# Kernel tuning notes

Measured on AMD Instinct MI355X. Metric: run time of the kernel, lower is better.

## Reference

```python
import jax, jax.numpy as jnp
import numpy as np

TOP_K = 64   # make_graph default top_k
KMIN = 9     # make_graph default kmin
EPS = 1e-6


def rbf(D):
    # matches rbf(): D_min=0, D_max=20, D_count=36
    D_mu = jnp.linspace(0.0, 20.0, 36)
    D_sigma = 20.0 / 36
    return jnp.exp(-(((D[..., None] - D_mu) / D_sigma) ** 2))


def setup_inputs() -> dict:
    key = jax.random.key(0)
    ks = jax.random.split(key, 6)
    B, L, E, Dn, Do = 1, 1536, 32, 32, 32
    # backbone coords (B, L, 3 atoms, 3); scaled so CA-CA distances span the RBF range
    xyz = jax.random.normal(ks[0], (B, L, 3, 3), jnp.float32) * 10.0
    pair = jax.random.normal(ks[1], (B, L, L, E), jnp.float32)   # embedded pair feats (num_edge_features)
    node = jax.random.normal(ks[2], (B, L, Dn), jnp.float32)      # l0 node features
    idx = jnp.broadcast_to(jnp.arange(L, dtype=jnp.int32), (B, L))  # residue indices
    W_e = jax.random.normal(ks[3], (E + 36, Do), jnp.float32) / np.sqrt(E + 36)
    W_n = jax.random.normal(ks[4], (Dn, Do), jnp.float32) / np.sqrt(Dn)
    w_gate = jax.random.normal(ks[5], (Do,), jnp.float32) / np.sqrt(Do)
    return {"xyz": xyz, "pair": pair, "node": node, "idx": idx,
            "W_e": W_e, "W_n": W_n, "w_gate": w_gate}


def reference(xyz, pair, node, idx, W_e, W_n, w_gate):
    B, L = xyz.shape[:2]
    ca = xyz[:, :, 1]                                   # (B,L,3) CA coords
    diff = ca[:, None, :, :] - ca[:, :, None, :]        # d_ij = ca_j - ca_i  (B,L,L,3)
    D = jnp.sqrt(jnp.sum(diff * diff, -1) + 1e-12)      # cdist (B,L,L)
    eye = jnp.eye(L, dtype=D.dtype)
    D_big = D + eye[None] * 999.9                       # mask self for kNN, as in make_graph
    sep = jnp.abs(idx[:, None, :] - idx[:, :, None]).astype(D.dtype) + eye[None] * 999.9

    # topk smallest distances -> scatter into dense adjacency, union with seq-sep < kmin
    k = min(TOP_K, L)
    _, E_idx = jax.lax.top_k(-D_big, k)                 # (B,L,k)
    topk = jnp.zeros((B, L, L), D.dtype).at[
        jnp.arange(B)[:, None, None], jnp.arange(L)[None, :, None], E_idx].set(1.0)
    mask = jnp.logical_or(topk > 0.0, sep < KMIN)       # (B,L,L) graph edges

    # per-edge features: pair feats ++ 36-dim RBF of CA distance
    edge_feat = jnp.concatenate([pair, rbf(D)], -1)     # (B,L,L,E+36)
    msg = jax.nn.relu(
        jnp.einsum('bijf,fo->bijo', edge_feat, W_e)
        + jnp.einsum('bjd,do->bjo', node, W_n)[:, None, :, :])
    msg = msg * mask[..., None]
    deg = jnp.sum(mask.astype(msg.dtype), -1, keepdims=True)   # (B,L,1)

    node_out = jnp.sum(msg, 2) / (deg + EPS)            # (B,L,Do) scalar output
    gate = jnp.einsum('bijo,o->bij', msg, w_gate)       # per-edge scalar gate
    # edge vectors are detached in make_graph (edata['d'] = (...).detach())
    diff_sg = jax.lax.stop_gradient(diff)
    vec_out = jnp.sum(gate[..., None] * diff_sg, 2) / (deg + EPS)  # (B,L,3) vector output
    return jnp.concatenate([node_out, vec_out], -1)     # (B,L,Do+3)
```

## Files before the change

kernel.cpp:

```cpp
#include <hip/hip_runtime.h>
#include <hip/hip_bf16.h>
#include <math.h>

#define L_MAX 1536
#define TOPK  64
#define KMIN  9

__launch_bounds__(256, 2)
__global__ void finalblock_kernel(
    const float* __restrict__ xyz,
    const float* __restrict__ pair,
    const float* __restrict__ node,
    const int*   __restrict__ idxg,
    const float* __restrict__ We,
    const float* __restrict__ Wn,
    const float* __restrict__ wg,
    float* __restrict__ out,
    int B, int L)
{
    const int tid = threadIdx.x;
    const int row = blockIdx.x;
    const int b = row / L;
    const int i = row - b * L;

    __shared__ float    ca[L_MAX * 3];
    __shared__ unsigned d2b[L_MAX];
    __shared__ float    We_s[68 * 32];
    __shared__ float    Wn_s[32 * 32];
    __shared__ float    wg_s[32];
    __shared__ float    feat[8][100];
    __shared__ int      elist[128];
    __shared__ float    red[8 * 32];
    __shared__ float    vred[8][3];
    __shared__ int      ecnt;
    __shared__ int      wsum[4];

    for (int t = tid; t < 68 * 32; t += 256) We_s[t] = We[t];
    for (int t = tid; t < 32 * 32; t += 256) Wn_s[t] = Wn[t];
    if (tid < 32) wg_s[tid] = wg[tid];
    for (int t = tid; t < L * 3; t += 256) {
        int j = t / 3, c = t - j * 3;
        ca[t] = xyz[((size_t)(b * L + j)) * 9 + 3 + c];
    }
    if (tid == 0) ecnt = 0;
    __syncthreads();

    const float cix = ca[i * 3 + 0], ciy = ca[i * 3 + 1], ciz = ca[i * 3 + 2];

    for (int j = tid; j < L; j += 256) {
        float dx = ca[j * 3 + 0] - cix;
        float dy = ca[j * 3 + 1] - ciy;
        float dz = ca[j * 3 + 2] - ciz;
        float d2 = dx * dx + dy * dy + dz * dz + 1e-12f;
        if (j == i) d2 = 3.0e38f;
        d2b[j] = __float_as_uint(d2);
    }
    __syncthreads();

    unsigned v[6];
    unsigned char alive = 0;
    int nv = 0;
    for (int j = tid; j < L; j += 256) { v[nv] = d2b[j]; alive |= (unsigned char)(1u << nv); nv++; }

    unsigned thr = 0;
    int kk = TOPK;
    for (int bit = 31; bit >= 0; --bit) {
        int cnt = 0; unsigned char c0 = 0;
        for (int e = 0; e < nv; e++) {
            if ((alive >> e) & 1) {
                if (!((v[e] >> bit) & 1u)) { c0 |= (unsigned char)(1u << e); cnt++; }
            }
        }
        for (int off = 32; off; off >>= 1) cnt += __shfl_xor(cnt, off, 64);
        if ((tid & 63) == 0) wsum[tid >> 6] = cnt;
        __syncthreads();
        int C = wsum[0] + wsum[1] + wsum[2] + wsum[3];
        __syncthreads();
        if (C >= kk) {
            alive &= c0;
        } else {
            kk -= C;
            alive = (unsigned char)(alive & ~c0);
            thr |= (1u << bit);
        }
    }

    const int idx_i = idxg[b * L + i];
    for (int j = tid; j < L; j += 256) {
        bool m = (d2b[j] <= thr);
        if (!m && j != i) {
            int s = idxg[b * L + j] - idx_i;
            s = s < 0 ? -s : s;
            m = (s < KMIN);
        }
        if (m) {
            int p = atomicAdd(&ecnt, 1);
            if (p < 128) elist[p] = j;
        }
    }
    __syncthreads();
    const int deg = ecnt < 128 ? ecnt : 128;

    const int slot = tid >> 5;
    const int o    = tid & 31;
    float node_acc = 0.f;
    float vx = 0.f, vy = 0.f, vz = 0.f;

    for (int base = 0; base < deg; base += 8) {
        __syncthreads();
        const int eg = base + slot;

        if (eg < deg) {
            int j = elist[eg];
            feat[slot][o]      = pair[((size_t)(b * L + i) * L + j) * 32 + o];
            feat[slot][68 + o] = node[((size_t)(b * L + j)) * 32 + o];
        } else {
            feat[slot][o] = 0.f;
            feat[slot][68 + o] = 0.f;
        }
        for (int q = tid; q < 8 * 36; q += 256) {
            int sl = q / 36, r = q - sl * 36;
            int eg2 = base + sl;
            float val = 0.f;
            if (eg2 < deg) {
                float Dv = sqrtf(__uint_as_float(d2b[elist[eg2]]));
                float t = (Dv - (float)r * (20.0f / 35.0f)) * (36.0f / 20.0f);
                val = __expf(-t * t);
            }
            feat[sl][32 + r] = val;
        }
        __syncthreads();

        float acc = 0.f;
        if (eg < deg) {
            #pragma unroll
            for (int f = 0; f < 68; f++) acc = fmaf(feat[slot][f], We_s[f * 32 + o], acc);
            #pragma unroll
            for (int d = 0; d < 32; d++) acc = fmaf(feat[slot][68 + d], Wn_s[d * 32 + o], acc);
            acc = fmaxf(acc, 0.f);
        }
        node_acc += acc;

        float g = acc * wg_s[o];
        for (int w = 16; w; w >>= 1) g += __shfl_xor(g, w, 32);
        if (o == 0 && eg < deg) {
            int j = elist[eg];
            vx += g * (ca[j * 3 + 0] - cix);
            vy += g * (ca[j * 3 + 1] - ciy);
            vz += g * (ca[j * 3 + 2] - ciz);
        }
    }

    red[slot * 32 + o] = node_acc;
    if (o == 0) { vred[slot][0] = vx; vred[slot][1] = vy; vred[slot][2] = vz; }
    __syncthreads();

    const float denom = (float)deg + 1e-6f;
    const size_t orow = (size_t)(b * L + i) * 35;
    if (tid < 32) {
        float s = 0.f;
        #pragma unroll
        for (int s8 = 0; s8 < 8; s8++) s += red[s8 * 32 + tid];
        out[orow + tid] = s / denom;
    } else if (tid < 35) {
        int c = tid - 32;
        float s = 0.f;
        #pragma unroll
        for (int s8 = 0; s8 < 8; s8++) s += vred[s8][c];
        out[orow + 32 + c] = s / denom;
    }
}

extern "C" void kernel_launch(void* const* d_in, const int* in_sizes, int n_in,
                              void* d_out, int out_size, void* d_ws, size_t ws_size,
                              hipStream_t stream) {
    const float* xyz  = (const float*)d_in[0];
    const float* pair = (const float*)d_in[1];
    const float* node = (const float*)d_in[2];
    const int*   idx  = (const int*)d_in[3];
    const float* We   = (const float*)d_in[4];
    const float* Wn   = (const float*)d_in[5];
    const float* wg   = (const float*)d_in[6];
    float* out = (float*)d_out;

    const int BL = in_sizes[3];
    const long pair_sz = (long)in_sizes[1];
    const int L = (int)(pair_sz / ((long)BL * 32));
    const int B = BL / L;

    finalblock_kernel<<<dim3(B * L), dim3(256), 0, stream>>>(
        xyz, pair, node, idx, We, Wn, wg, out, B, L);
}
```

Baseline: 464.0 us.

## Process one row per wavefront with ballot-based radix top-k and register weights

Each 256-thread block now handles four rows, one wavefront per row, instead of one row per block. The radix select uses wave ballots with no block barriers and exits early once the remaining candidates exactly fill k. The edge list is built by ballot prefix instead of shared atomics, weights are held in registers, and the next edge's features are prefetched during compute. The cost is heavy register pressure from the 100-float weight column plus 24 distance values. The per-row state also assumes all four rows in a block share the same batch index.

```diff
diff --git a/kernel.cpp b/kernel.cpp
--- a/kernel.cpp
+++ b/kernel.cpp
@@ -5,6 +5,9 @@
 #define L_MAX 1536
 #define TOPK  64
 #define KMIN  9
+#define RPB   4
+#define NV    24
+#define MAXE  128
 
 __launch_bounds__(256, 2)
 __global__ void finalblock_kernel(
@@ -18,156 +21,206 @@
     float* __restrict__ out,
     int B, int L)
 {
-    const int tid = threadIdx.x;
-    const int row = blockIdx.x;
-    const int b = row / L;
-    const int i = row - b * L;
-
-    __shared__ float    ca[L_MAX * 3];
-    __shared__ unsigned d2b[L_MAX];
-    __shared__ float    We_s[68 * 32];
-    __shared__ float    Wn_s[32 * 32];
-    __shared__ float    wg_s[32];
-    __shared__ float    feat[8][100];
-    __shared__ int      elist[128];
-    __shared__ float    red[8 * 32];
-    __shared__ float    vred[8][3];
-    __shared__ int      ecnt;
-    __shared__ int      wsum[4];
-
-    for (int t = tid; t < 68 * 32; t += 256) We_s[t] = We[t];
-    for (int t = tid; t < 32 * 32; t += 256) Wn_s[t] = Wn[t];
-    if (tid < 32) wg_s[tid] = wg[tid];
+    const int tid  = threadIdx.x;
+    const int lane = tid & 63;
+    const int w    = tid >> 6;
+    const int row  = blockIdx.x * RPB + w;
+    const int BL   = B * L;
+
+    __shared__ float ca[L_MAX * 3];
+    __shared__ alignas(16) float feat[RPB][2][104];
+    __shared__ int   elist[RPB][MAXE];
+    __shared__ float ed2[RPB][MAXE];
+
+    const int b0 = (blockIdx.x * RPB) / L;
     for (int t = tid; t < L * 3; t += 256) {
         int j = t / 3, c = t - j * 3;
-        ca[t] = xyz[((size_t)(b * L + j)) * 9 + 3 + c];
-    }
-    if (tid == 0) ecnt = 0;
+        ca[t] = xyz[((size_t)(b0 * L + j)) * 9 + 3 + c];
+    }
     __syncthreads();
 
-    const float cix = ca[i * 3 + 0], ciy = ca[i * 3 + 1], ciz = ca[i * 3 + 2];
-
-    for (int j = tid; j < L; j += 256) {
-        float dx = ca[j * 3 + 0] - cix;
-        float dy = ca[j * 3 + 1] - ciy;
-        float dz = ca[j * 3 + 2] - ciz;
-        float d2 = dx * dx + dy * dy + dz * dz + 1e-12f;
-        if (j == i) d2 = 3.0e38f;
-        d2b[j] = __float_as_uint(d2);
-    }
-    __syncthreads();
-
-    unsigned v[6];
-    unsigned char alive = 0;
-    int nv = 0;
-    for (int j = tid; j < L; j += 256) { v[nv] = d2b[j]; alive |= (unsigned char)(1u << nv); nv++; }
-
-    unsigned thr = 0;
+    if (row >= BL) return;
+    const int i = row - b0 * L;
+    const int gbase = b0 * L;
+    const int o = lane & 31;
+    const int e2 = lane >> 5;
+
+    const float ci0 = ca[i * 3 + 0], ci1 = ca[i * 3 + 1], ci2 = ca[i * 3 + 2];
+
+    unsigned vbits[NV];
+    unsigned aliveInit = 0u;
+    #pragma unroll
+    for (int t = 0; t < NV; ++t) {
+        int j = lane + (t << 6);
+        unsigned ub = 0x7F7FFFFFu;
+        if (j < L) {
+            float dx = ca[j * 3 + 0] - ci0;
+            float dy = ca[j * 3 + 1] - ci1;
+            float dz = ca[j * 3 + 2] - ci2;
+            float d2 = dx * dx + dy * dy + dz * dz + 1e-12f;
+            if (j == i) d2 = 3.0e38f;
+            ub = __float_as_uint(d2);
+            aliveInit |= (1u << t);
+        }
+        vbits[t] = ub;
+    }
+
+    unsigned thr = 0u;
+    unsigned alive = aliveInit;
     int kk = TOPK;
-    for (int bit = 31; bit >= 0; --bit) {
-        int cnt = 0; unsigned char c0 = 0;
-        for (int e = 0; e < nv; e++) {
-            if ((alive >> e) & 1) {
-                if (!((v[e] >> bit) & 1u)) { c0 |= (unsigned char)(1u << e); cnt++; }
-            }
-        }
-        for (int off = 32; off; off >>= 1) cnt += __shfl_xor(cnt, off, 64);
-        if ((tid & 63) == 0) wsum[tid >> 6] = cnt;
-        __syncthreads();
-        int C = wsum[0] + wsum[1] + wsum[2] + wsum[3];
-        __syncthreads();
-        if (C >= kk) {
-            alive &= c0;
-        } else {
-            kk -= C;
-            alive = (unsigned char)(alive & ~c0);
-            thr |= (1u << bit);
-        }
-    }
-
-    const int idx_i = idxg[b * L + i];
-    for (int j = tid; j < L; j += 256) {
-        bool m = (d2b[j] <= thr);
-        if (!m && j != i) {
-            int s = idxg[b * L + j] - idx_i;
-            s = s < 0 ? -s : s;
-            m = (s < KMIN);
-        }
+    int aliveCnt = L;
+    for (int bit = 30; bit >= 0; --bit) {
+        unsigned c0 = 0u;
+        int cnt = 0;
+        #pragma unroll
+        for (int t = 0; t < NV; ++t) {
+            bool z = ((alive >> t) & 1u) && !((vbits[t] >> bit) & 1u);
+            unsigned long long blt = __ballot((int)z);
+            cnt += __popcll(blt);
+            if (z) c0 |= (1u << t);
+        }
+        if (cnt >= kk) { alive &= c0; aliveCnt = cnt; }
+        else { kk -= cnt; aliveCnt -= cnt; alive &= ~c0; thr |= (1u << bit); }
+        if (aliveCnt == kk) {
+            unsigned mx = 0u;
+            #pragma unroll
+            for (int t = 0; t < NV; ++t)
+                if ((alive >> t) & 1u) mx = vbits[t] > mx ? vbits[t] : mx;
+            #pragma unroll
+            for (int off = 32; off; off >>= 1) {
+                unsigned m2 = (unsigned)__shfl_xor((int)mx, off, 64);
+                mx = m2 > mx ? m2 : mx;
+            }
+            thr = mx;
+            break;
+        }
+    }
+
+    const int idx_i = idxg[gbase + i];
+    int cnt = 0;
+    #pragma unroll
+    for (int t = 0; t < NV; ++t) {
+        int j = lane + (t << 6);
+        bool m = false;
+        if (j < L) {
+            m = (vbits[t] <= thr);
+            if (!m && j != i) {
+                int s = idxg[gbase + j] - idx_i;
+                s = s < 0 ? -s : s;
+                m = (s < KMIN);
+            }
+        }
+        unsigned long long blt = __ballot((int)m);
         if (m) {
-            int p = atomicAdd(&ecnt, 1);
-            if (p < 128) elist[p] = j;
-        }
-    }
-    __syncthreads();
-    const int deg = ecnt < 128 ? ecnt : 128;
-
-    const int slot = tid >> 5;
-    const int o    = tid & 31;
-    float node_acc = 0.f;
-    float vx = 0.f, vy = 0.f, vz = 0.f;
-
-    for (int base = 0; base < deg; base += 8) {
-        __syncthreads();
-        const int eg = base + slot;
-
-        if (eg < deg) {
-            int j = elist[eg];
-            feat[slot][o]      = pair[((size_t)(b * L + i) * L + j) * 32 + o];
-            feat[slot][68 + o] = node[((size_t)(b * L + j)) * 32 + o];
-        } else {
-            feat[slot][o] = 0.f;
-            feat[slot][68 + o] = 0.f;
-        }
-        for (int q = tid; q < 8 * 36; q += 256) {
-            int sl = q / 36, r = q - sl * 36;
-            int eg2 = base + sl;
+            int pos = cnt + __popcll(blt & ((1ull << lane) - 1ull));
+            if (pos < MAXE) {
+                elist[w][pos] = j;
+                ed2[w][pos] = __uint_as_float(vbits[t]);
+            }
+        }
+        cnt += __popcll(blt);
+    }
+    const int deg = cnt < MAXE ? cnt : MAXE;
+    asm volatile("s_waitcnt lgkmcnt(0)" ::: "memory");
+    __builtin_amdgcn_wave_barrier();
+
+    float wcol[100];
+    #pragma unroll
+    for (int f = 0; f < 68; ++f) wcol[f] = We[f * 32 + o];
+    #pragma unroll
+    for (int d = 0; d < 32; ++d) wcol[68 + d] = Wn[d * 32 + o];
+    const float wgo = wg[o];
+
+    float node_acc = 0.f, vxa = 0.f, vya = 0.f, vza = 0.f;
+    const int nst = (deg + 1) >> 1;
+
+    float pv = 0.f, nv = 0.f, dvv = 0.f;
+    {
+        int e = e2;
+        if (e < deg) {
+            int j = elist[w][e];
+            pv = pair[((size_t)(gbase + i) * L + j) * 32 + o];
+            nv = node[((size_t)(gbase + j)) * 32 + o];
+            if (o < 3) dvv = ca[j * 3 + o] - ca[i * 3 + o];
+        }
+    }
+
+    for (int s = 0; s < nst; ++s) {
+        feat[w][e2][o]      = pv;
+        feat[w][e2][68 + o] = nv;
+        if (o < 3) feat[w][e2][100 + o] = dvv;
+        {
+            int e = (lane >= 36) ? 1 : 0;
+            int r = lane - e * 36;
+            int eg = 2 * s + e;
             float val = 0.f;
-            if (eg2 < deg) {
-                float Dv = sqrtf(__uint_as_float(d2b[elist[eg2]]));
-                float t = (Dv - (float)r * (20.0f / 35.0f)) * (36.0f / 20.0f);
-                val = __expf(-t * t);
-            }
-            feat[sl][32 + r] = val;
-        }
-        __syncthreads();
-
+            if (eg < deg) {
+                float D = sqrtf(ed2[w][eg]);
+                float tt = (D - (float)r * (20.0f / 35.0f)) * 1.8f;
+                val = __expf(-tt * tt);
+            }
+            feat[w][e][32 + r] = val;
+            if (lane < 8) {
+                int r2 = lane + 28;
+                int eg2 = 2 * s + 1;
+                float v2 = 0.f;
+                if (eg2 < deg) {
+                    float D = sqrtf(ed2[w][eg2]);
+                    float tt = (D - (float)r2 * (20.0f / 35.0f)) * 1.8f;
+                    v2 = __expf(-tt * tt);
+                }
+                feat[w][1][32 + r2] = v2;
+            }
+        }
+        asm volatile("s_waitcnt lgkmcnt(0)" ::: "memory");
+        __builtin_amdgcn_wave_barrier();
+
+        pv = 0.f; nv = 0.f; dvv = 0.f;
+        if (s + 1 < nst) {
+            int e = 2 * (s + 1) + e2;
+            if (e < deg) {
+                int j = elist[w][e];
+                pv = pair[((size_t)(gbase + i) * L + j) * 32 + o];
+                nv = node[((size_t)(gbase + j)) * 32 + o];
+                if (o < 3) dvv = ca[j * 3 + o] - ca[i * 3 + o];
+            }
+        }
+
+        const float* fb = &feat[w][e2][0];
         float acc = 0.f;
-        if (eg < deg) {
-            #pragma unroll
-            for (int f = 0; f < 68; f++) acc = fmaf(feat[slot][f], We_s[f * 32 + o], acc);
-            #pragma unroll
-            for (int d = 0; d < 32; d++) acc = fmaf(feat[slot][68 + d], Wn_s[d * 32 + o], acc);
-            acc = fmaxf(acc, 0.f);
-        }
+        #pragma unroll
+        for (int f4 = 0; f4 < 25; ++f4) {
+            float4 fv = *reinterpret_cast<const float4*>(fb + f4 * 4);
+            acc = fmaf(fv.x, wcol[f4 * 4 + 0], acc);
+            acc = fmaf(fv.y, wcol[f4 * 4 + 1], acc);
+            acc = fmaf(fv.z, wcol[f4 * 4 + 2], acc);
+            acc = fmaf(fv.w, wcol[f4 * 4 + 3], acc);
+        }
+        acc = fmaxf(acc, 0.f);
         node_acc += acc;
 
-        float g = acc * wg_s[o];
-        for (int w = 16; w; w >>= 1) g += __shfl_xor(g, w, 32);
-        if (o == 0 && eg < deg) {
-            int j = elist[eg];
-            vx += g * (ca[j * 3 + 0] - cix);
-            vy += g * (ca[j * 3 + 1] - ciy);
-            vz += g * (ca[j * 3 + 2] - ciz);
-        }
-    }
-
-    red[slot * 32 + o] = node_acc;
-    if (o == 0) { vred[slot][0] = vx; vred[slot][1] = vy; vred[slot][2] = vz; }
-    __syncthreads();
-
+        float g = acc * wgo;
+        float dx = fb[100], dy = fb[101], dz = fb[102];
+        vxa = fmaf(g, dx, vxa);
+        vya = fmaf(g, dy, vya);
+        vza = fmaf(g, dz, vza);
+        __builtin_amdgcn_wave_barrier();
+    }
+
+    node_acc += __shfl_xor(node_acc, 32, 64);
+    #pragma unroll
+    for (int off = 32; off; off >>= 1) {
+        vxa += __shfl_xor(vxa, off, 64);
+        vya += __shfl_xor(vya, off, 64);
+        vza += __shfl_xor(vza, off, 64);
+    }
     const float denom = (float)deg + 1e-6f;
-    const size_t orow = (size_t)(b * L + i) * 35;
-    if (tid < 32) {
-        float s = 0.f;
-        #pragma unroll
-        for (int s8 = 0; s8 < 8; s8++) s += red[s8 * 32 + tid];
-        out[orow + tid] = s / denom;
-    } else if (tid < 35) {
-        int c = tid - 32;
-        float s = 0.f;
-        #pragma unroll
-        for (int s8 = 0; s8 < 8; s8++) s += vred[s8][c];
-        out[orow + 32 + c] = s / denom;
+    const size_t orow = (size_t)row * 35;
+    if (lane < 32) out[orow + lane] = node_acc / denom;
+    if (lane == 0) {
+        out[orow + 32] = vxa / denom;
+        out[orow + 33] = vya / denom;
+        out[orow + 34] = vza / denom;
     }
 }
 
@@ -188,6 +241,7 @@
     const int L = (int)(pair_sz / ((long)BL * 32));
     const int B = BL / L;
 
-    finalblock_kernel<<<dim3(B * L), dim3(256), 0, stream>>>(
+    const int grid = (BL + RPB - 1) / RPB;
+    finalblock_kernel<<<dim3(grid), dim3(256), 0, stream>>>(
         xyz, pair, node, idx, We, Wn, wg, out, B, L);
 }
```

Measured after the change: 409.2 us. 11.8% less time.
